# Optimization experiments

Measured on AMD Instinct MI355X. Metric: run time of the kernel, lower is better.

The kernel has to match this reference:

```python
import jax, jax.numpy as jnp
import numpy as np

CONF_THRES = 0.596
IOU_THRES = 0.45
MAX_WH = 4096.0
K_CAND = 512      # NMS candidate cap (static)
MAX_DET = 300     # padded detections per image
IMG = 768.0       # hw = x[1].shape[-2:] * 8 -> 96*8


def _bilinear(feat, y, x):
    # feat: [C,H,W]; y,x: [R,S] sample coords. torchvision-style bilinear w/ border handling.
    C, H, W = feat.shape
    valid = (y > -1.0) & (y < H) & (x > -1.0) & (x < W)
    y = jnp.clip(y, 0.0)
    x = jnp.clip(x, 0.0)
    y0 = jnp.minimum(jnp.floor(y), H - 1).astype(jnp.int32)
    x0 = jnp.minimum(jnp.floor(x), W - 1).astype(jnp.int32)
    y1 = jnp.minimum(y0 + 1, H - 1)
    x1 = jnp.minimum(x0 + 1, W - 1)
    ly = y - y0
    lx = x - x0
    hy = 1.0 - ly
    hx = 1.0 - lx
    f00 = feat[:, y0, x0]
    f01 = feat[:, y0, x1]
    f10 = feat[:, y1, x0]
    f11 = feat[:, y1, x1]
    val = hy * hx * f00 + hy * lx * f01 + ly * hx * f10 + ly * lx * f11
    return val * valid  # [C,R,S]


def _roi_align_1x1(feat, boxes, scale):
    # RoIAlign(output_size=1, aligned=False); adaptive sampling_ratio replaced by fixed 2x2 grid.
    b = boxes * scale
    x1, y1, x2, y2 = b[:, 0], b[:, 1], b[:, 2], b[:, 3]
    rw = jnp.maximum(x2 - x1, 1.0)
    rh = jnp.maximum(y2 - y1, 1.0)
    offs = jnp.array([0.25, 0.75], dtype=boxes.dtype)  # (i+0.5)/2
    ys = y1[:, None] + rh[:, None] * offs  # [R,2]
    xs = x1[:, None] + rw[:, None] * offs
    R = ys.shape[0]
    yy = jnp.broadcast_to(ys[:, :, None], (R, 2, 2)).reshape(R, 4)
    xx = jnp.broadcast_to(xs[:, None, :], (R, 2, 2)).reshape(R, 4)
    v = _bilinear(feat, yy, xx)  # [C,R,4]
    return v.mean(-1).T  # [R,C]


def _iou_matrix(b):
    area = (b[:, 2] - b[:, 0]) * (b[:, 3] - b[:, 1])
    lt = jnp.maximum(b[:, None, :2], b[None, :, :2])
    rb = jnp.minimum(b[:, None, 2:], b[None, :, 2:])
    wh = jnp.clip(rb - lt, 0.0)
    inter = wh[..., 0] * wh[..., 1]
    return inter / (area[:, None] + area[None, :] - inter + 1e-7)


def _nms_image(pred):
    # pred: [N, 5+nc]. yolov5 non_max_suppression, static-shape version.
    obj = pred[:, 4]
    conf_all = pred[:, 5:] * obj[:, None]
    conf = conf_all.max(-1)
    cls = jnp.argmax(conf_all, -1)
    xy = pred[:, :2]
    wh = pred[:, 2:4]
    boxes = jnp.concatenate([xy - wh / 2, xy + wh / 2], -1)  # xywh2xyxy
    valid = (obj > CONF_THRES) & (conf > CONF_THRES)
    score = jnp.where(valid, conf, 0.0)
    sc, idx = jax.lax.top_k(score, K_CAND)
    b = boxes[idx]
    c = cls[idx].astype(boxes.dtype)
    iou = _iou_matrix(b + c[:, None] * MAX_WH)  # per-class offset NMS
    ar = jnp.arange(K_CAND)

    def body(i, keep):
        sup = keep[i] & (iou[i] > IOU_THRES) & (ar > i)
        return keep & (~sup)

    keep = jax.lax.fori_loop(0, K_CAND, body, sc > 0.0)
    sc2 = jnp.where(keep, sc, 0.0)
    sc3, idx2 = jax.lax.top_k(sc2, MAX_DET)
    return b[idx2], sc3 > 0.0  # [MAX_DET,4], [MAX_DET]


def _per_image(pred, g1, g2, g3, g4, W1, b1, W2, b2):
    bbox, mask = _nms_image(pred)
    f = jnp.concatenate([
        _roi_align_1x1(g1, bbox, 1.0 / 8),
        _roi_align_1x1(g2, bbox, 1.0 / 16),
        _roi_align_1x1(g3, bbox, 1.0 / 32),
        _roi_align_1x1(g4, bbox, 1.0 / 64),
    ], axis=1)  # [MAX_DET, 1920]
    h = jax.nn.leaky_relu(f @ W1 + b1)
    h = jax.nn.leaky_relu(h @ W2 + b2)
    out = jnp.concatenate([bbox / IMG, h], axis=-1)  # [MAX_DET, 4+64]
    return out * mask[:, None].astype(out.dtype)


def setup_inputs() -> dict:
    key = jax.random.key(0)
    ks = jax.random.split(key, 9)
    B, N, NC = 8, 36720, 80
    r = jax.random.uniform(ks[0], (B, N, 5 + NC), dtype=jnp.float32)
    xy = r[..., :2] * IMG
    wh = r[..., 2:4] * 112.0 + 8.0
    preds = jnp.concatenate([xy, wh, r[..., 4:]], axis=-1)
    f1 = jax.random.normal(ks[1], (B, 128, 96, 96), dtype=jnp.float32)
    f2 = jax.random.normal(ks[2], (B, 256, 48, 48), dtype=jnp.float32)
    f3 = jax.random.normal(ks[3], (B, 512, 24, 24), dtype=jnp.float32)
    f4 = jax.random.normal(ks[4], (B, 1024, 12, 12), dtype=jnp.float32)
    W1 = jax.random.normal(ks[5], (1920, 64), dtype=jnp.float32) / np.sqrt(1920.0)
    b1 = jnp.zeros((64,), jnp.float32)
    W2 = jax.random.normal(ks[6], (64, 64), dtype=jnp.float32) / 8.0
    b2 = jnp.zeros((64,), jnp.float32)
    return {"preds": preds, "f1": f1, "f2": f2, "f3": f3, "f4": f4,
            "W1": W1, "b1": b1, "W2": W2, "b2": b2}


def reference(preds, f1, f2, f3, f4, W1, b1, W2, b2):
    fn = lambda p, a, b_, c, d: _per_image(p, a, b_, c, d, W1, b1, W2, b2)
    return jax.vmap(fn)(preds, f1, f2, f3, f4)  # [B, MAX_DET, 68]
```

## Files before the change

kernel.cpp:

```cpp
#include <hip/hip_runtime.h>
#include <cstdint>

#define B_IMG   8
#define NCAND   36720
#define PD      85
#define NCLS    80
#define KC      512
#define MAXDET  300
#define NBUCK   2048
#define CANDCAP 1024

#define G2_OFF 4718592
#define G3_OFF 5898240
#define G4_OFF 6193152
#define G_TOT  6266880

#define P2_BASE 0
#define P2_SLAB 1179648
#define P3_BASE 2359296
#define P3_SLAB 294912
#define P4_BASE 3538944
#define P4_SLAB 73728

typedef unsigned int u32;
typedef unsigned long long u64;

__device__ __forceinline__ float leaky(float x){ return x >= 0.f ? x : 0.01f*x; }

__device__ __forceinline__ u64 shfl_u64(u64 v, int lane){
  int lo = __shfl((int)(u32)(v & 0xFFFFFFFFull), lane, 64);
  int hi = __shfl((int)(u32)(v >> 32), lane, 64);
  return ((u64)(u32)hi << 32) | (u64)(u32)lo;
}
__device__ __forceinline__ u64 shfl_xor_u64(u64 v, int mask){
  int lo = __shfl_xor((int)(u32)(v & 0xFFFFFFFFull), mask, 64);
  int hi = __shfl_xor((int)(u32)(v >> 32), mask, 64);
  return ((u64)(u32)hi << 32) | (u64)(u32)lo;
}

__global__ __launch_bounds__(256) void k_score(const float* __restrict__ preds,
    u32* __restrict__ sbits, int* __restrict__ clsArr, u32* __restrict__ hist){
  __shared__ u32   sl_lane[4][64];
  __shared__ float sl_obj[4][64];
  __shared__ u32   sl_res[4][64];
  __shared__ u32   sl_cls[4][64];
  const int img  = blockIdx.y;
  const int wv   = threadIdx.x >> 6;
  const int lane = threadIdx.x & 63;
  const int base = (blockIdx.x*4 + wv)*64;
  const int ci   = base + lane;
  const bool inb = ci < NCAND;
  float obj = 0.f;
  if (inb) obj = preds[((long)img*NCAND + ci)*PD + 4];
  const bool pass = obj > 0.596f;
  u64 mask = __ballot(pass);
  int cnt  = __popcll(mask);
  int rank = __popcll(mask & ((1ull << lane) - 1ull));
  if (pass){ sl_lane[wv][rank] = (u32)lane; sl_obj[wv][rank] = obj; }
  const int q = lane & 3;
  for (int r0 = 0; r0 < cnt; r0 += 16){
    int idx = r0 + (lane >> 2);
    if (idx < cnt){
      u32 sl = sl_lane[wv][idx];
      float obj2 = sl_obj[wv][idx];
      const float* p2 = preds + ((long)img*NCAND + base + (int)sl)*PD + 5 + q;
      u64 best = 0ull;
      #pragma unroll
      for (int k = 0; k < 20; k++){
        float v = p2[4*k] * obj2;
        u64 key = ((u64)__float_as_uint(v) << 32) | (u64)(~(u32)(q + 4*k));
        if (key > best) best = key;
      }
      u64 o1 = shfl_xor_u64(best, 1); if (o1 > best) best = o1;
      u64 o2 = shfl_xor_u64(best, 2); if (o2 > best) best = o2;
      if (q == 0){
        u32 bits = (u32)(best >> 32);
        sl_res[wv][sl] = (__uint_as_float(bits) > 0.596f) ? bits : 0u;
        sl_cls[wv][sl] = ~(u32)(best & 0xFFFFFFFFull);
      }
    }
  }
  if (inb){
    u32 out = pass ? sl_res[wv][lane] : 0u;
    sbits[(long)img*NCAND + ci] = out;
    if (pass) clsArr[(long)img*NCAND + ci] = (int)sl_cls[wv][lane];
    if (out) atomicAdd(&hist[img*NBUCK + ((out - 0x3F000000u) >> 12)], 1u);
  }
}

__global__ __launch_bounds__(64) void k_thresh(const u32* __restrict__ hist,
                                               u32* __restrict__ thr){
  const int img = blockIdx.x;
  const int lane = threadIdx.x;
  const u32* h = hist + img*NBUCK;
  u32 acc = 0; u32 result = 0x3F000000u; bool found = false;
  for (int g = NBUCK/64 - 1; g >= 0 && !found; g--){
    u32 v = h[g*64 + lane];
    u32 s = v;
    #pragma unroll
    for (int off = 1; off < 64; off <<= 1){
      u32 t = __shfl_down(s, off, 64);
      s += (lane + off < 64) ? t : 0u;
    }
    u64 mask = __ballot(acc + s >= KC);
    if (mask){
      int hl = 63 - __clzll(mask);
      result = 0x3F000000u + ((u32)(g*64 + hl) << 12);
      found = true;
    }
    acc += __shfl(s, 0, 64);
  }
  if (lane == 0) thr[img] = result;
}

__global__ __launch_bounds__(256) void k_gather(const u32* __restrict__ sbits,
    const u32* __restrict__ thr, u32* __restrict__ cnt, u64* __restrict__ cand){
  int img = blockIdx.y;
  int n = blockIdx.x*256 + threadIdx.x;
  if (n >= NCAND) return;
  u32 bits = sbits[(long)img*NCAND + n];
  if (bits && bits >= thr[img]){
    u32 pos = atomicAdd(&cnt[img], 1u);
    if (pos < CANDCAP)
      cand[(long)img*CANDCAP + pos] = ((u64)bits << 32) | (u64)(0xFFFFFFFFu - (u32)n);
  }
}

__global__ __launch_bounds__(256) void k_rank(const float* __restrict__ preds,
    const int* __restrict__ clsArr, const u64* __restrict__ cand,
    const u32* __restrict__ cnt, float4* __restrict__ cbs_g,
    float4* __restrict__ obs_g, u64* __restrict__ kmask_g){
#pragma clang fp contract(off)
  __shared__ __align__(16) u64 keys[CANDCAP];
  const int img = blockIdx.x >> 2;
  const int sub = blockIdx.x & 3;
  const int tid = threadIdx.x;
  const int M = min((int)cnt[img], CANDCAP);
  #pragma unroll
  for (int k = 0; k < 4; k++){
    int s = k*256 + tid;
    keys[s] = (s < M) ? cand[(long)img*CANDCAP + s] : 0ull;
  }
  __syncthreads();
  const int slot = sub*256 + tid;
  u64 k0 = keys[slot];
  int r0 = 0;
  const ulonglong2* kv = (const ulonglong2*)keys;
  for (int j = 0; j < CANDCAP/2; j++){
    ulonglong2 kk = kv[j];
    r0 += (kk.x > k0) + (kk.y > k0);
  }
  if ((k0 >> 32) != 0ull && r0 < KC){
    u32 idxn = 0xFFFFFFFFu - (u32)(k0 & 0xFFFFFFFFull);
    const float* p = preds + ((long)img*NCAND + idxn)*PD;
    float cx = p[0], cy = p[1], w = p[2], h = p[3];
    float hw = w*0.5f, hh = h*0.5f;
    float X1 = cx-hw, Y1 = cy-hh, X2 = cx+hw, Y2 = cy+hh;
    float off = (float)clsArr[(long)img*NCAND + idxn] * 4096.0f;
    obs_g[(long)img*KC + r0] = make_float4(X1, Y1, X2, Y2);
    cbs_g[(long)img*KC + r0] = make_float4(X1+off, Y1+off, X2+off, Y2+off);
    atomicOr(&kmask_g[img*8 + (r0 >> 6)], 1ull << (r0 & 63));
  }
}

__global__ __launch_bounds__(512) void k_iou(const float4* __restrict__ cbs_g,
    const u64* __restrict__ kmask_g, u64* __restrict__ lrows_g){
#pragma clang fp contract(off)
  __shared__ __align__(16) float4 cbsL[8*65];
  const int img = blockIdx.x >> 3;
  const int ch  = blockIdx.x & 7;
  const int tid = threadIdx.x;
  if (tid < KC){
    u64 km = kmask_g[img*8 + (tid >> 6)];
    bool f = (km >> (tid & 63)) & 1ull;
    float4 v = f ? cbs_g[(long)img*KC + tid]
                 : make_float4(-4e8f, -4e8f, -4e8f, -4e8f);
    cbsL[(tid >> 6)*65 + (tid & 63)] = v;
  }
  __syncthreads();
  const int row = ch*64 + (tid >> 3);
  const int w   = tid & 7;
  float4 bi = cbsL[(row >> 6)*65 + (row & 63)];
  float areai = (bi.z - bi.x)*(bi.w - bi.y);
  u64 bits = 0ull;
  const int jbase = w*64;
  for (int b = 0; b < 64; b++){
    int j = jbase + b;
    if (j > row){
      float4 bj = cbsL[w*65 + b];
      float areaj = (bj.z - bj.x)*(bj.w - bj.y);
      float ltx = fmaxf(bi.x, bj.x), lty = fmaxf(bi.y, bj.y);
      float rbx = fminf(bi.z, bj.z), rby = fminf(bi.w, bj.w);
      float ww = fmaxf(rbx - ltx, 0.f);
      float hh = fmaxf(rby - lty, 0.f);
      float inter = ww*hh;
      float iou = inter / (areai + areaj - inter + 1e-7f);
      if (iou > 0.45f) bits |= (1ull << b);
    }
  }
  lrows_g[((long)img*KC + row)*8 + w] = bits;
}

__global__ __launch_bounds__(512) void k_greedy(const u64* __restrict__ lrows_g,
    const u64* __restrict__ kmask_g, const float4* __restrict__ obs_g,
    float* __restrict__ selbox, u32* __restrict__ selcnt){
  __shared__ __align__(16) u64 lrows[KC*8];
  __shared__ u64 keepw[8];
  const int img = blockIdx.x;
  const int tid = threadIdx.x;
  const ulonglong2* src = (const ulonglong2*)(lrows_g + (long)img*KC*8);
  ulonglong2* dst = (ulonglong2*)lrows;
  #pragma unroll
  for (int k = 0; k < 4; k++) dst[k*512 + tid] = src[k*512 + tid];
  __syncthreads();
  if (tid < 64){
    const int lane = tid;
    const int w = lane & 7;
    u64 kw_own = kmask_g[img*8 + w];
    for (int b = 0; b < 8; b++){
      u64 kwb = shfl_u64(kw_own, b);
      for (int g = 0; g < 8; g++){
        u64 rdec[8], rown[8];
        #pragma unroll
        for (int k = 0; k < 8; k++){
          int i = b*64 + g*8 + k;
          rdec[k] = lrows[i*8 + b];
          rown[k] = lrows[i*8 + w];
        }
        #pragma unroll
        for (int k = 0; k < 8; k++){
          int il = g*8 + k;
          if ((kwb >> il) & 1ull){
            kwb    &= ~rdec[k];
            kw_own &= ~rown[k];
          }
        }
      }
    }
    if (lane < 8) keepw[lane] = kw_own;
  }
  __syncthreads();
  {
    u64 kk[8];
    #pragma unroll
    for (int w = 0; w < 8; w++) kk[w] = keepw[w];
    const int s = tid;
    const int wi = s >> 6, bi = s & 63;
    bool kept = (kk[wi] >> bi) & 1ull;
    if (kept){
      int rank = 0;
      for (int w = 0; w < wi; w++) rank += __popcll(kk[w]);
      rank += __popcll(bi ? (kk[wi] & ((1ull << bi) - 1ull)) : 0ull);
      if (rank < MAXDET){
        float4 ob = obs_g[(long)img*KC + s];
        float* sb = selbox + ((long)img*MAXDET + rank)*4;
        sb[0]=ob.x; sb[1]=ob.y; sb[2]=ob.z; sb[3]=ob.w;
      }
    }
    if (tid == 0){
      int tot = 0;
      #pragma unroll
      for (int w = 0; w < 8; w++) tot += __popcll(kk[w]);
      selcnt[img] = (u32)min(tot, MAXDET);
    }
  }
}

__device__ __forceinline__ void load_chunk(const float4* __restrict__ feat4,
    const float4* __restrict__ W14, long fbase, int hw4, int px04, int Woff,
    int c0, int tid, float4 (&rF)[4], float4 (&rW)[2]){
  #pragma unroll
  for (int k = 0; k < 4; k++){
    int s = tid + k*256; int c = s >> 5, q = s & 31;
    int pq = px04 + q; if (pq >= hw4) pq = hw4 - 1;
    rF[k] = feat4[fbase + (long)(c0 + c)*hw4 + pq];
  }
  #pragma unroll
  for (int k = 0; k < 2; k++){
    int s = tid + k*256; int c = s >> 4, q = s & 15;
    rW[k] = W14[(long)(Woff + c0 + c)*16 + q];
  }
}

#define FMA_ROW(S, A) \
  A.x = fmaf(S, wv.x, A.x); A.y = fmaf(S, wv.y, A.y); \
  A.z = fmaf(S, wv.z, A.z); A.w = fmaf(S, wv.w, A.w);

__global__ __launch_bounds__(256, 2) void k_proj(const float* __restrict__ f1,
    const float* __restrict__ f2, const float* __restrict__ f3,
    const float* __restrict__ f4, const float* __restrict__ W1,
    float* __restrict__ G, float* __restrict__ P){
  __shared__ __align__(16) float Fs[32*128];
  __shared__ __align__(16) float Ws[32*64];
  const int img = blockIdx.y;
  const int u   = blockIdx.x;
  const float* feat; int C, HW, Woff, tile, split; long pbase; bool multi;
  if (u < 16)      { feat=f4; C=1024; HW=144;  Woff=896; tile=u>>3;      split=u&7;
                     pbase=P4_BASE + (long)split*P4_SLAB; multi=true;  }
  else if (u < 36) { feat=f3; C=512;  HW=576;  Woff=384; tile=(u-16)>>2; split=(u-16)&3;
                     pbase=P3_BASE + (long)split*P3_SLAB; multi=true;  }
  else if (u < 72) { feat=f2; C=256;  HW=2304; Woff=128; tile=(u-36)>>1; split=(u-36)&1;
                     pbase=P2_BASE + (long)split*P2_SLAB; multi=true;  }
  else             { feat=f1; C=128;  HW=9216; Woff=0;   tile=u-72;      split=0;
                     pbase=0; multi=false; }
  const int px0  = tile*128;
  const int hw4  = HW >> 2;
  const int px04 = px0 >> 2;
  const int tid  = threadIdx.x;
  const int jg   = tid & 15;
  const int pg   = tid >> 4;
  const int c0b  = split*128;
  const float4* feat4 = (const float4*)feat;
  const float4* W14   = (const float4*)W1;
  float4* Fs4 = (float4*)Fs;
  float4* Ws4 = (float4*)Ws;
  const long fbase = (long)img*C*hw4;
  float4 rF[4]; float4 rW[2];
  float4 a0 = make_float4(0.f,0.f,0.f,0.f), a1 = a0, a2 = a0, a3 = a0;
  float4 a4 = a0, a5 = a0, a6 = a0, a7 = a0;

  load_chunk(feat4, W14, fbase, hw4, px04, Woff, c0b, tid, rF, rW);
  for (int ch = 0; ch < 4; ch++){
    __syncthreads();
    #pragma unroll
    for (int k = 0; k < 4; k++) Fs4[tid + k*256] = rF[k];
    #pragma unroll
    for (int k = 0; k < 2; k++) Ws4[tid + k*256] = rW[k];
    if (ch < 3)
      load_chunk(feat4, W14, fbase, hw4, px04, Woff, c0b + (ch+1)*32, tid, rF, rW);
    __syncthreads();
    #pragma unroll 8
    for (int c = 0; c < 32; c++){
      float4 fa = Fs4[c*32 + pg*2];
      float4 fb = Fs4[c*32 + pg*2 + 1];
      float4 wv = Ws4[c*16 + jg];
      FMA_ROW(fa.x, a0) FMA_ROW(fa.y, a1) FMA_ROW(fa.z, a2) FMA_ROW(fa.w, a3)
      FMA_ROW(fb.x, a4) FMA_ROW(fb.y, a5) FMA_ROW(fb.z, a6) FMA_ROW(fb.w, a7)
    }
  }
  float* outb = multi ? (P + pbase + (long)img*HW*64)
                      : (G + (long)img*HW*64);
  const int pxa = px0 + pg*8;
#define STOREQ(A, PP) do { int gp = pxa + (PP); if (gp < HW){ \
    *(float4*)(outb + (long)gp*64 + jg*4) = A; } } while(0)
  STOREQ(a0, 0); STOREQ(a1, 1); STOREQ(a2, 2); STOREQ(a3, 3);
  STOREQ(a4, 4); STOREQ(a5, 5); STOREQ(a6, 6); STOREQ(a7, 7);
#undef STOREQ
}

__global__ __launch_bounds__(256) void k_reduce(const float4* __restrict__ P4f,
                                                float4* __restrict__ G4f){
  const int N2 = P2_SLAB/4;
  const int N3 = P3_SLAB/4;
  const int N4 = P4_SLAB/4;
  int t = blockIdx.x*256 + threadIdx.x;
  if (t < N2){
    float4 a = P4f[t];
    float4 b = P4f[N2 + t];
    float4 r = make_float4(a.x+b.x, a.y+b.y, a.z+b.z, a.w+b.w);
    G4f[G2_OFF/4 + t] = r;
  } else if (t < N2 + N3){
    int u = t - N2;
    const float4* base = P4f + P3_BASE/4 + u;
    float4 r = base[0];
    #pragma unroll
    for (int s = 1; s < 4; s++){
      float4 b = base[(long)s*N3];
      r.x += b.x; r.y += b.y; r.z += b.z; r.w += b.w;
    }
    G4f[G3_OFF/4 + u] = r;
  } else if (t < N2 + N3 + N4){
    int u = t - N2 - N3;
    const float4* base = P4f + P4_BASE/4 + u;
    float4 r = base[0];
    #pragma unroll
    for (int s = 1; s < 8; s++){
      float4 b = base[(long)s*N4];
      r.x += b.x; r.y += b.y; r.z += b.z; r.w += b.w;
    }
    G4f[G4_OFF/4 + u] = r;
  }
}

__device__ __forceinline__ void roi_level(const float* __restrict__ g,
    int Hl, int Wl, float scale, float x1, float y1, float x2, float y2,
    int lane, float& h){
  float bx1=x1*scale, by1=y1*scale, bx2=x2*scale, by2=y2*scale;
  float rw=fmaxf(bx2-bx1,1.f), rh=fmaxf(by2-by1,1.f);
  float ys[2]={by1+rh*0.25f, by1+rh*0.75f};
  float xs[2]={bx1+rw*0.25f, bx1+rw*0.75f};
  #pragma unroll
  for (int pt = 0; pt < 4; pt++){
    float y=ys[pt>>1], x=xs[pt&1];
    if ((y>-1.f)&&(y<(float)Hl)&&(x>-1.f)&&(x<(float)Wl)){
      float yc=fmaxf(y,0.f), xc=fmaxf(x,0.f);
      int y0=(int)fminf(floorf(yc),(float)(Hl-1));
      int x0=(int)fminf(floorf(xc),(float)(Wl-1));
      int y1i=min(y0+1,Hl-1), x1i=min(x0+1,Wl-1);
      float ly=yc-(float)y0, lx=xc-(float)x0;
      float hy=1.f-ly, hx=1.f-lx;
      h += (hy*hx*0.25f)*g[(long)(y0*Wl+x0)*64+lane];
      h += (hy*lx*0.25f)*g[(long)(y0*Wl+x1i)*64+lane];
      h += (ly*hx*0.25f)*g[(long)(y1i*Wl+x0)*64+lane];
      h += (ly*lx*0.25f)*g[(long)(y1i*Wl+x1i)*64+lane];
    }
  }
}

__global__ __launch_bounds__(256) void k_roi_mlp(const float* __restrict__ G,
    const float* __restrict__ selbox, const u32* __restrict__ selcnt,
    const float* __restrict__ b1, const float* __restrict__ W2,
    const float* __restrict__ b2, float* __restrict__ out){
  const int img  = blockIdx.y;
  const int wave = threadIdx.x >> 6;
  const int lane = threadIdx.x & 63;
  const int slot = blockIdx.x*4 + wave;
  if (slot >= MAXDET) return;
  float* o = out + ((long)img*MAXDET + slot)*68;
  if (slot >= (int)selcnt[img]){
    o[4+lane] = 0.f;
    if (lane < 4) o[lane] = 0.f;
    return;
  }
  const float* sb = selbox + ((long)img*MAXDET + slot)*4;
  float x1 = sb[0], y1 = sb[1], x2 = sb[2], y2 = sb[3];
  const float* Gi1 = G +          (long)img*9216*64;
  const float* Gi2 = G + G2_OFF + (long)img*2304*64;
  const float* Gi3 = G + G3_OFF + (long)img*576*64;
  const float* Gi4 = G + G4_OFF + (long)img*144*64;
  float h = 0.f;
  roi_level(Gi1, 96, 96, 0.125f,    x1,y1,x2,y2, lane, h);
  roi_level(Gi2, 48, 48, 0.0625f,   x1,y1,x2,y2, lane, h);
  roi_level(Gi3, 24, 24, 0.03125f,  x1,y1,x2,y2, lane, h);
  roi_level(Gi4, 12, 12, 0.015625f, x1,y1,x2,y2, lane, h);
  float h1 = leaky(h + b1[lane]);
  float c = 0.f;
  #pragma unroll 8
  for (int k = 0; k < 64; k++){
    float hk = __shfl(h1, k, 64);
    c += hk * W2[k*64 + lane];
  }
  o[4+lane] = leaky(c + b2[lane]);
  if (lane < 4) o[lane] = sb[lane] / 768.0f;
}

#define WS_G 2914048
#define WS_P 27981568

extern "C" void kernel_launch(void* const* d_in, const int* in_sizes, int n_in,
                              void* d_out, int out_size, void* d_ws, size_t ws_size,
                              hipStream_t stream){
  const float* preds = (const float*)d_in[0];
  const float* f1 = (const float*)d_in[1];
  const float* f2 = (const float*)d_in[2];
  const float* f3 = (const float*)d_in[3];
  const float* f4 = (const float*)d_in[4];
  const float* W1 = (const float*)d_in[5];
  const float* b1 = (const float*)d_in[6];
  const float* W2 = (const float*)d_in[7];
  const float* b2 = (const float*)d_in[8];
  float* out = (float*)d_out;
  char* ws = (char*)d_ws;
  u32* hist    = (u32*)(ws + 0);
  u32* cnt     = (u32*)(ws + 65536);
  u64* kmask_g = (u64*)(ws + 65792);
  u32* thr     = (u32*)(ws + 66304);
  float* selb  = (float*)(ws + 66560);
  u32* selc    = (u32*)(ws + 104960);
  u32* sbits   = (u32*)(ws + 105216);
  int* clsA    = (int*)(ws + 1280256);
  u64* cand    = (u64*)(ws + 2455296);
  float4* cbs_g = (float4*)(ws + 2520832);
  float4* obs_g = (float4*)(ws + 2586368);
  u64* lrows_g  = (u64*)(ws + 2651904);
  float* G     = (float*)(ws + WS_G);
  float* P     = (float*)(ws + WS_P);

  hipMemsetAsync(ws, 0, 66304, stream);

  dim3 gs((NCAND + 255)/256, B_IMG);
  k_score<<<gs, 256, 0, stream>>>(preds, sbits, clsA, hist);
  k_thresh<<<B_IMG, 64, 0, stream>>>(hist, thr);
  dim3 g3((NCAND+255)/256, B_IMG);
  k_gather<<<g3, 256, 0, stream>>>(sbits, thr, cnt, cand);
  k_rank<<<B_IMG*4, 256, 0, stream>>>(preds, clsA, cand, cnt, cbs_g, obs_g, kmask_g);
  k_iou<<<B_IMG*8, 512, 0, stream>>>(cbs_g, kmask_g, lrows_g);
  k_greedy<<<B_IMG, 512, 0, stream>>>(lrows_g, kmask_g, obs_g, selb, selc);
  k_proj<<<dim3(144, B_IMG), 256, 0, stream>>>(f1, f2, f3, f4, W1, G, P);
  k_reduce<<<1512, 256, 0, stream>>>((const float4*)P, (float4*)G);
  k_roi_mlp<<<dim3((MAXDET+3)/4, B_IMG), 256, 0, stream>>>(G, selb, selc, b1, W2, b2, out);
}
```

Baseline: 358.4 us.

## Stage projection tiles directly into double-buffered LDS via global_load_lds

The feature and weight tile loads in the projection kernel now use direct global-to-LDS loads into a double buffer, replacing register staging followed by LDS stores. This removes the register round trip and one barrier per chunk, and lets the next chunk load while the current one is computed. The occupancy hint of two blocks per CU is dropped, and LDS use per block doubles. Correctness depends on the asynchronous LDS loads being complete by the barrier, since no explicit vmcnt wait is visible.

```diff
diff --git a/kernel.cpp b/kernel.cpp
--- a/kernel.cpp
+++ b/kernel.cpp
@@ -266,19 +266,25 @@
   }
 }
 
-__device__ __forceinline__ void load_chunk(const float4* __restrict__ feat4,
+__device__ __forceinline__ void gld16(const void* g, void* l){
+  __builtin_amdgcn_global_load_lds((const __attribute__((address_space(1))) void*)g,
+                                   (__attribute__((address_space(3))) void*)l, 16, 0, 0);
+}
+
+__device__ __forceinline__ void stage_chunk(const float4* __restrict__ feat4,
     const float4* __restrict__ W14, long fbase, int hw4, int px04, int Woff,
-    int c0, int tid, float4 (&rF)[4], float4 (&rW)[2]){
+    int c0, int tid, float4* FsD, float4* WsD){
+  const int wb = tid & ~63;
   #pragma unroll
   for (int k = 0; k < 4; k++){
     int s = tid + k*256; int c = s >> 5, q = s & 31;
     int pq = px04 + q; if (pq >= hw4) pq = hw4 - 1;
-    rF[k] = feat4[fbase + (long)(c0 + c)*hw4 + pq];
+    gld16(feat4 + fbase + (long)(c0 + c)*hw4 + pq, FsD + k*256 + wb);
   }
   #pragma unroll
   for (int k = 0; k < 2; k++){
     int s = tid + k*256; int c = s >> 4, q = s & 15;
-    rW[k] = W14[(long)(Woff + c0 + c)*16 + q];
+    gld16(W14 + (long)(Woff + c0 + c)*16 + q, WsD + k*256 + wb);
   }
 }
 
@@ -286,12 +292,12 @@
   A.x = fmaf(S, wv.x, A.x); A.y = fmaf(S, wv.y, A.y); \
   A.z = fmaf(S, wv.z, A.z); A.w = fmaf(S, wv.w, A.w);
 
-__global__ __launch_bounds__(256, 2) void k_proj(const float* __restrict__ f1,
+__global__ __launch_bounds__(256) void k_proj(const float* __restrict__ f1,
     const float* __restrict__ f2, const float* __restrict__ f3,
     const float* __restrict__ f4, const float* __restrict__ W1,
     float* __restrict__ G, float* __restrict__ P){
-  __shared__ __align__(16) float Fs[32*128];
-  __shared__ __align__(16) float Ws[32*64];
+  __shared__ __align__(16) float Fs[2][32*128];
+  __shared__ __align__(16) float Ws[2][32*64];
   const int img = blockIdx.y;
   const int u   = blockIdx.x;
   const float* feat; int C, HW, Woff, tile, split; long pbase; bool multi;
@@ -312,31 +318,28 @@
   const int c0b  = split*128;
   const float4* feat4 = (const float4*)feat;
   const float4* W14   = (const float4*)W1;
-  float4* Fs4 = (float4*)Fs;
-  float4* Ws4 = (float4*)Ws;
   const long fbase = (long)img*C*hw4;
-  float4 rF[4]; float4 rW[2];
   float4 a0 = make_float4(0.f,0.f,0.f,0.f), a1 = a0, a2 = a0, a3 = a0;
   float4 a4 = a0, a5 = a0, a6 = a0, a7 = a0;
 
-  load_chunk(feat4, W14, fbase, hw4, px04, Woff, c0b, tid, rF, rW);
+  stage_chunk(feat4, W14, fbase, hw4, px04, Woff, c0b, tid,
+              (float4*)Fs[0], (float4*)Ws[0]);
+  __syncthreads();
   for (int ch = 0; ch < 4; ch++){
-    __syncthreads();
-    #pragma unroll
-    for (int k = 0; k < 4; k++) Fs4[tid + k*256] = rF[k];
-    #pragma unroll
-    for (int k = 0; k < 2; k++) Ws4[tid + k*256] = rW[k];
     if (ch < 3)
-      load_chunk(feat4, W14, fbase, hw4, px04, Woff, c0b + (ch+1)*32, tid, rF, rW);
-    __syncthreads();
+      stage_chunk(feat4, W14, fbase, hw4, px04, Woff, c0b + (ch+1)*32, tid,
+                  (float4*)Fs[(ch+1)&1], (float4*)Ws[(ch+1)&1]);
+    const float4* fsb = (const float4*)Fs[ch&1];
+    const float4* wsb = (const float4*)Ws[ch&1];
     #pragma unroll 8
     for (int c = 0; c < 32; c++){
-      float4 fa = Fs4[c*32 + pg*2];
-      float4 fb = Fs4[c*32 + pg*2 + 1];
-      float4 wv = Ws4[c*16 + jg];
+      float4 fa = fsb[c*32 + pg*2];
+      float4 fb = fsb[c*32 + pg*2 + 1];
+      float4 wv = wsb[c*16 + jg];
       FMA_ROW(fa.x, a0) FMA_ROW(fa.y, a1) FMA_ROW(fa.z, a2) FMA_ROW(fa.w, a3)
       FMA_ROW(fb.x, a4) FMA_ROW(fb.y, a5) FMA_ROW(fb.z, a6) FMA_ROW(fb.w, a7)
     }
+    __syncthreads();
   }
   float* outb = multi ? (P + pbase + (long)img*HW*64)
                       : (G + (long)img*HW*64);
```

Measured after the change: 331.3 us. 1.08x faster.
